# Kernel tuning notes

Measured on AMD Instinct MI355X. Metric: run time of the kernel, lower is better.

## Reference

```python
import jax, jax.numpy as jnp
import numpy as np

B, N, DIM = 4, 1024, 1024
HEADS, DH = 16, 64
INNER = HEADS * DH          # 1024
PROJ_H = max(16, DH // 8)   # 16
TOP_K = 256
TEMP = 1.0
SCALE = DH ** -0.5
LN_EPS = 1e-5


def setup_inputs() -> dict:
    key = jax.random.key(0)
    ks = jax.random.split(key, 9)
    s = 0.02
    return {
        "x": jax.random.normal(ks[0], (B, N, DIM), dtype=jnp.float32),
        "w_qkv": jax.random.normal(ks[1], (3 * INNER, DIM), dtype=jnp.float32) * s,
        "w_out": jax.random.normal(ks[2], (DIM, INNER), dtype=jnp.float32) * s,
        "b_out": jnp.zeros((DIM,), dtype=jnp.float32),
        "ln_g": jnp.ones((DH,), dtype=jnp.float32),
        "ln_b": jnp.zeros((DH,), dtype=jnp.float32),
        "w1": jax.random.normal(ks[3], (PROJ_H, DH), dtype=jnp.float32) * s,
        "b1": jnp.zeros((PROJ_H,), dtype=jnp.float32),
        "w2": jax.random.normal(ks[4], (1, PROJ_H), dtype=jnp.float32) * s,
        "b2": jnp.zeros((1,), dtype=jnp.float32),
    }


def _soma_gate(token_feat, ln_g, ln_b, w1, b1, w2, b2):
    # token_feat: [B, N, DH] -> gate [B, N] in (0,1)
    mu = token_feat.mean(axis=-1, keepdims=True)
    var = token_feat.var(axis=-1, keepdims=True)
    H = (token_feat - mu) * jax.lax.rsqrt(var + LN_EPS) * ln_g + ln_b
    h = jax.nn.gelu(H @ w1.T + b1, approximate=False)
    scores = (h @ w2.T + b2)[..., 0]                       # [B, N]
    scores = scores / (TEMP + 1e-12)
    # top-k soft mask: non-topk positions set to -1e9 before sigmoid
    topk_vals, topk_idx = jax.lax.top_k(scores, TOP_K)
    b_idx = jnp.arange(scores.shape[0])[:, None]
    scores = jnp.full_like(scores, -1e9).at[b_idx, topk_idx].set(topk_vals)
    return jax.nn.sigmoid(scores)


def reference(x, w_qkv, w_out, b_out, ln_g, ln_b, w1, b1, w2, b2):
    Bx, Nx, _ = x.shape
    qkv = x @ w_qkv.T                                      # [B, N, 3*INNER]
    q, k, v = jnp.split(qkv, 3, axis=-1)
    to_heads = lambda t: t.reshape(Bx, Nx, HEADS, DH).transpose(0, 2, 1, 3)
    q, k, v = to_heads(q), to_heads(k), to_heads(v)        # [B, H, N, DH]

    dots = jnp.einsum('bhid,bhjd->bhij', q, k) * SCALE     # [B, H, N, N]

    q_mean = q.mean(axis=1)                                # [B, N, DH]
    gate = _soma_gate(q_mean, ln_g, ln_b, w1, b1, w2, b2)  # [B, N]
    dots = dots * (gate[:, None, :, None] * gate[:, None, None, :])

    attn = jax.nn.softmax(dots, axis=-1)
    out = jnp.einsum('bhij,bhjd->bhid', attn, v)           # [B, H, N, DH]
    out = out.transpose(0, 2, 1, 3).reshape(Bx, Nx, INNER)
    return out @ w_out.T + b_out
```

## Files before the change

### kernel.cpp

```cpp
#include <hip/hip_runtime.h>
#include <hip/hip_bf16.h>
#include <stdint.h>

typedef __bf16 bf16;
typedef __bf16 bf16x8 __attribute__((ext_vector_type(8)));
typedef float floatx4 __attribute__((ext_vector_type(4)));

typedef const __attribute__((address_space(1))) uint32_t glb_u32;
typedef __attribute__((address_space(3))) uint32_t lds_u32;

__device__ __forceinline__ void cp16(void* lds, const void* gp) {
    __builtin_amdgcn_global_load_lds((glb_u32*)gp, (lds_u32*)lds, 16, 0, 0);
}

#define MFMA16(a, b, c) __builtin_amdgcn_mfma_f32_16x16x32_bf16((a), (b), (c), 0, 0, 0)
#define SCALE_ 0.125f

__global__ __launch_bounds__(256) void k_cvt_prep(
    const float* __restrict__ x, const float* __restrict__ wq,
    const float* __restrict__ wo, bf16* __restrict__ xb,
    bf16* __restrict__ xl, bf16* __restrict__ wqb, bf16* __restrict__ wob,
    bf16* __restrict__ whl, float* __restrict__ xsum) {
    __shared__ float red[4][64];
    if (blockIdx.x < 4096) {
        size_t i8 = ((size_t)blockIdx.x * 256 + threadIdx.x) * 8;
        const float* src; bf16* dst; size_t off; bool isx = false;
        if (i8 < 4194304)      { src = x;  dst = xb;  off = i8; isx = true; }
        else if (i8 < 7340032) { src = wq; dst = wqb; off = i8 - 4194304; }
        else                   { src = wo; dst = wob; off = i8 - 7340032; }
        float4 a = *(const float4*)(src + off);
        float4 b = *(const float4*)(src + off + 4);
        union { bf16 h[8]; uint4 u; } hi, lo;
        hi.h[0] = (bf16)a.x; hi.h[1] = (bf16)a.y; hi.h[2] = (bf16)a.z; hi.h[3] = (bf16)a.w;
        hi.h[4] = (bf16)b.x; hi.h[5] = (bf16)b.y; hi.h[6] = (bf16)b.z; hi.h[7] = (bf16)b.w;
        *(uint4*)(dst + off) = hi.u;
        if (isx) {
            lo.h[0] = (bf16)(a.x - (float)hi.h[0]);
            lo.h[1] = (bf16)(a.y - (float)hi.h[1]);
            lo.h[2] = (bf16)(a.z - (float)hi.h[2]);
            lo.h[3] = (bf16)(a.w - (float)hi.h[3]);
            lo.h[4] = (bf16)(b.x - (float)hi.h[4]);
            lo.h[5] = (bf16)(b.y - (float)hi.h[5]);
            lo.h[6] = (bf16)(b.z - (float)hi.h[6]);
            lo.h[7] = (bf16)(b.w - (float)hi.h[7]);
            *(uint4*)(xl + off) = lo.u;
        }
    } else if (blockIdx.x < 4352) {
        int t = (blockIdx.x - 4096) * 256 + threadIdx.x;
        int k = t & 1023, d = t >> 10;
        float s = 0.f;
        #pragma unroll
        for (int h = 0; h < 16; ++h) s += wq[(size_t)(h * 64 + d) * 1024 + k];
        s *= (1.f / 16.f);
        bf16 hi = (bf16)s;
        whl[(size_t)d * 1024 + k] = hi;
        whl[(size_t)(64 + d) * 1024 + k] = (bf16)(s - (float)hi);
    } else {
        int j = blockIdx.x - 4352;
        int b = j >> 4, c0 = (j & 15) << 6;
        int lane = threadIdx.x & 63, q = threadIdx.x >> 6;
        const float* p = x + (size_t)b * 1048576 + (size_t)q * 262144 + c0 + lane;
        float s = 0.f;
        #pragma unroll 8
        for (int n = 0; n < 256; ++n) s += p[(size_t)n * 1024];
        red[q][lane] = s;
        __syncthreads();
        if (threadIdx.x < 64)
            xsum[b * 1024 + c0 + threadIdx.x] =
                red[0][threadIdx.x] + red[1][threadIdx.x] +
                red[2][threadIdx.x] + red[3][threadIdx.x];
    }
}

__global__ __launch_bounds__(256) void k_score_gemm(
    const bf16* __restrict__ xh, const bf16* __restrict__ xl,
    const bf16* __restrict__ whl, float* __restrict__ qm8) {
    __shared__ bf16 Ah[64 * 32];
    __shared__ bf16 Al[64 * 32];
    __shared__ bf16 Bs[128 * 32];
    const int t = threadIdx.x;
    const int lane = t & 63;
    const int w = t >> 6;
    const int m0 = (blockIdx.x >> 3) * 64;
    const int kbase = (blockIdx.x & 7) * 128;
    const int srow = t >> 2;
    const int scol = (t & 3) * 8;
    const int fr = lane & 15;
    const int kc = (lane >> 4) * 8;

    floatx4 zero4 = {0.f, 0.f, 0.f, 0.f};
    floatx4 acc[4] = {zero4, zero4, zero4, zero4};

    for (int k0 = kbase; k0 < kbase + 128; k0 += 32) {
        __syncthreads();
        cp16(Ah + t * 8,        xh + (size_t)(m0 + srow) * 1024 + k0 + scol);
        cp16(Al + t * 8,        xl + (size_t)(m0 + srow) * 1024 + k0 + scol);
        cp16(Bs + t * 8,        whl + (size_t)srow * 1024 + k0 + scol);
        cp16(Bs + t * 8 + 2048, whl + (size_t)(srow + 64) * 1024 + k0 + scol);
        __syncthreads();
        bf16x8 ah, al, bh[4], bl[4];
        ah = *(const bf16x8*)&Ah[(w * 16 + fr) * 32 + kc];
        al = *(const bf16x8*)&Al[(w * 16 + fr) * 32 + kc];
        #pragma unroll
        for (int ni = 0; ni < 4; ++ni) {
            bh[ni] = *(const bf16x8*)&Bs[(ni * 16 + fr) * 32 + kc];
            bl[ni] = *(const bf16x8*)&Bs[(64 + ni * 16 + fr) * 32 + kc];
        }
        #pragma unroll
        for (int ni = 0; ni < 4; ++ni) {
            acc[ni] = MFMA16(ah, bh[ni], acc[ni]);
            acc[ni] = MFMA16(ah, bl[ni], acc[ni]);
            acc[ni] = MFMA16(al, bh[ni], acc[ni]);
        }
    }

    const int rowb = (lane >> 4) * 4;
    const size_t kofs = (size_t)(blockIdx.x & 7) * 4096;
    #pragma unroll
    for (int ni = 0; ni < 4; ++ni)
        #pragma unroll
        for (int r = 0; r < 4; ++r)
            qm8[(kofs + m0 + w * 16 + rowb + r) * 64 + ni * 16 + fr] = acc[ni][r];
}

__global__ __launch_bounds__(256) void k_score_tail(
    const float* __restrict__ qm8, const float* __restrict__ lng,
    const float* __restrict__ lnb, const float* __restrict__ w1f,
    const float* __restrict__ b1f, const float* __restrict__ w2f,
    const float* __restrict__ b2f, float* __restrict__ scores) {
    const int w = threadIdx.x >> 6, lane = threadIdx.x & 63;
    const int r = blockIdx.x * 4 + w;
    __shared__ float Hs[4][64];
    __shared__ float hh[4][16];

    float qm = 0.f;
    #pragma unroll
    for (int ks = 0; ks < 8; ++ks)
        qm += qm8[((size_t)ks * 4096 + r) * 64 + lane];
    float s = qm;
    #pragma unroll
    for (int off = 32; off > 0; off >>= 1) s += __shfl_xor(s, off);
    float mu = s * (1.f / 64.f);
    float dx = qm - mu;
    float v2 = dx * dx;
    #pragma unroll
    for (int off = 32; off > 0; off >>= 1) v2 += __shfl_xor(v2, off);
    float var = v2 * (1.f / 64.f);
    float H = dx * (1.0f / sqrtf(var + 1e-5f)) * lng[lane] + lnb[lane];
    Hs[w][lane] = H;
    if (lane < 16) {
        float a = b1f[lane];
        #pragma unroll
        for (int d = 0; d < 64; ++d) a += Hs[w][d] * w1f[lane * 64 + d];
        hh[w][lane] = 0.5f * a * (1.0f + erff(a * 0.70710678118654752f));
    }
    if (lane == 0) {
        float sc = b2f[0];
        #pragma unroll
        for (int p = 0; p < 16; ++p) sc += hh[w][p] * w2f[p];
        scores[r] = sc;
    }
}

__global__ __launch_bounds__(256) void k_topk(const float* __restrict__ scores,
                                              float* __restrict__ gate,
                                              int* __restrict__ idx,
                                              float* __restrict__ gsel) {
    const int w = threadIdx.x >> 6, lane = threadIdx.x & 63;
    const float* sc = scores + w * 1024;
    float s[16];
    uint32_t key[16];
    #pragma unroll
    for (int i = 0; i < 16; ++i) {
        s[i] = sc[lane * 16 + i];
        uint32_t u = __float_as_uint(s[i]);
        key[i] = (u >> 31) ? ~u : (u | 0x80000000u);
    }
    uint32_t prefix = 0;
    for (int bit = 31; bit >= 0; --bit) {
        uint32_t cand = prefix | (1u << bit);
        int c = 0;
        #pragma unroll
        for (int i = 0; i < 16; ++i) c += (key[i] >= cand);
        #pragma unroll
        for (int off = 1; off < 64; off <<= 1) c += __shfl_xor(c, off);
        if (c >= 256) prefix = cand;
    }
    int cg = 0, eq = 0;
    #pragma unroll
    for (int i = 0; i < 16; ++i) { cg += (key[i] > prefix); eq += (key[i] == prefix); }
    #pragma unroll
    for (int off = 1; off < 64; off <<= 1) cg += __shfl_xor(cg, off);
    const int quota = 256 - cg;
    int xs = eq;
    #pragma unroll
    for (int off = 1; off < 64; off <<= 1) {
        int y = __shfl_up(xs, off);
        if (lane >= off) xs += y;
    }
    int run = xs - eq;
    bool selv[16];
    int cnt = 0;
    #pragma unroll
    for (int i = 0; i < 16; ++i) {
        bool sel = key[i] > prefix;
        if (key[i] == prefix) { sel = (run < quota); run++; }
        selv[i] = sel;
        cnt += sel ? 1 : 0;
        gate[w * 1024 + lane * 16 + i] = sel ? 1.0f / (1.0f + expf(-s[i])) : 0.0f;
    }
    int xc = cnt;
    #pragma unroll
    for (int off = 1; off < 64; off <<= 1) {
        int y = __shfl_up(xc, off);
        if (lane >= off) xc += y;
    }
    int pos = xc - cnt;
    #pragma unroll
    for (int i = 0; i < 16; ++i) {
        if (selv[i]) {
            idx[w * 256 + pos]  = lane * 16 + i;
            gsel[w * 256 + pos] = 1.0f / (1.0f + expf(-s[i]));
            pos++;
        }
    }
}

__global__ __launch_bounds__(256) void k_qkv_sel(
    const bf16* __restrict__ xb, const bf16* __restrict__ wqb,
    const int* __restrict__ idx, bf16* __restrict__ qsel,
    bf16* __restrict__ ksel, bf16* __restrict__ VselT,
    const float* __restrict__ xsum, float* __restrict__ meanVbuf) {
    __shared__ bf16 As[64 * 32];
    __shared__ bf16 Bs[128 * 32];
    __shared__ float xsS[1024];
    const int t = threadIdx.x;

    if (blockIdx.x >= 384) {
        const int j = blockIdx.x - 384, b = j >> 2, kq = j & 3;
        for (int k = t; k < 1024; k += 256) xsS[k] = xsum[b * 1024 + k];
        __syncthreads();
        const int k2 = kq * 256 + t;
        const bf16* wr = wqb + (size_t)(2048 + k2) * 1024;
        float s = 0.f;
        for (int k = 0; k < 1024; k += 8) {
            bf16x8 v = *(const bf16x8*)(wr + k);
            #pragma unroll
            for (int jj = 0; jj < 8; ++jj) s += (float)v[jj] * xsS[k + jj];
        }
        meanVbuf[b * 1024 + k2] = s * (1.f / 1024.f);
        return;
    }

    const int lane = t & 63;
    const int w = t >> 6;
    const int srow = t >> 2;
    const int scol = (t & 3) * 8;
    const int fr = lane & 15;
    const int kc = (lane >> 4) * 8;

    const int bid = blockIdx.x;
    const int n0 = (bid % 24) * 128;
    const int m0 = (bid / 24) * 64;
    const bf16* Bsrc = wqb + (size_t)n0 * 1024;
    const int mg1 = m0 + srow;
    const int tok1 = idx[(mg1 >> 8) * 256 + (mg1 & 255)];
    const size_t abase1 = ((size_t)(mg1 >> 8) * 1024 + tok1) * 1024;

    floatx4 zero4 = {0.f, 0.f, 0.f, 0.f};
    floatx4 acc[4][2];
    #pragma unroll
    for (int i = 0; i < 4; ++i)
        #pragma unroll
        for (int j = 0; j < 2; ++j) acc[i][j] = zero4;

    for (int k0 = 0; k0 < 1024; k0 += 32) {
        __syncthreads();
        cp16(As + t * 8,        xb + abase1 + k0 + scol);
        cp16(Bs + t * 8,        Bsrc + (size_t)srow * 1024 + k0 + scol);
        cp16(Bs + t * 8 + 2048, Bsrc + (size_t)(srow + 64) * 1024 + k0 + scol);
        __syncthreads();
        bf16x8 a[4], b[2];
        #pragma unroll
        for (int mi = 0; mi < 4; ++mi)
            a[mi] = *(const bf16x8*)&As[(mi * 16 + fr) * 32 + kc];
        #pragma unroll
        for (int ni = 0; ni < 2; ++ni)
            b[ni] = *(const bf16x8*)&Bs[(w * 32 + ni * 16 + fr) * 32 + kc];
        #pragma unroll
        for (int mi = 0; mi < 4; ++mi)
            #pragma unroll
            for (int ni = 0; ni < 2; ++ni)
                acc[mi][ni] = MFMA16(a[mi], b[ni], acc[mi][ni]);
    }

    const int rowb = (lane >> 4) * 4;
    #pragma unroll
    for (int ni = 0; ni < 2; ++ni) {
        const int n_base = n0 + w * 32 + ni * 16;
        const int region = n_base >> 10;
        const int nn = n_base & 1023;
        const int h = nn >> 6;
        const int dd = (nn & 63) + fr;
        if (region < 2) {
            #pragma unroll
            for (int mi = 0; mi < 4; ++mi)
                #pragma unroll
                for (int r = 0; r < 4; ++r) {
                    const int mg = m0 + mi * 16 + rowb + r;
                    const bf16 v = (bf16)acc[mi][ni][r];
                    if (region == 0) {
                        qsel[(size_t)mg * 1024 + h * 64 + dd] = v;
                    } else {
                        const int b = mg >> 8, s = mg & 255;
                        ksel[(((size_t)(b * 16 + h)) * 256 + s) * 64 + dd] = v;
                    }
                }
        } else {
            #pragma unroll
            for (int mi = 0; mi < 4; ++mi) {
                const int mgb = m0 + mi * 16 + rowb;
                const int b = mgb >> 8, s0 = mgb & 255;
                union { bf16 h4[4]; uint2 u; } pk;
                #pragma unroll
                for (int r = 0; r < 4; ++r) pk.h4[r] = (bf16)acc[mi][ni][r];
                *(uint2*)&VselT[(((size_t)(b * 16 + h)) * 64 + dd) * 256 + s0] = pk.u;
            }
        }
    }
}

__global__ __launch_bounds__(256) void k_attn(
    bf16* __restrict__ qsel, const bf16* __restrict__ Ksel,
    const bf16* __restrict__ VselT, const float* __restrict__ gsel,
    const float* __restrict__ meanVbuf, const bf16* __restrict__ wob,
    const float* __restrict__ b_out, float* __restrict__ ubase) {
    __shared__ bf16 Qs[64 * 72];
    __shared__ bf16 Ks[64 * 72];
    __shared__ bf16 Vs[64 * 72];
    __shared__ bf16 Ps[4][16 * 72];
    __shared__ float redS[4][64];
    __shared__ float SumV[64];
    __shared__ float mvS[1024];
    const int t = threadIdx.x;

    if (blockIdx.x >= 256) {
        const int j = blockIdx.x - 256, bb = j >> 2, nq = j & 3;
        for (int k = t; k < 1024; k += 256) mvS[k] = meanVbuf[bb * 1024 + k];
        __syncthreads();
        const int n = nq * 256 + t;
        const bf16* wr = wob + (size_t)n * 1024;
        float s = b_out[n];
        for (int k = 0; k < 1024; k += 8) {
            bf16x8 v = *(const bf16x8*)(wr + k);
            #pragma unroll
            for (int jj = 0; jj < 8; ++jj) s += (float)v[jj] * mvS[k + jj];
        }
        ubase[bb * 1024 + n] = s;
        return;
    }

    const int bh = blockIdx.x >> 2;
    const int qt = blockIdx.x & 3;
    const int b = bh >> 4, h = bh & 15;
    const int w = t >> 6, lane = t & 63;
    const int m0 = qt * 64;
    const bf16* kb = Ksel + (size_t)bh * 16384;
    const bf16* vb = VselT + (size_t)bh * 16384;

    #pragma unroll
    for (int c = 0; c < 2; ++c) {
        int idx2 = t + 256 * c, row = idx2 >> 3, c8 = (idx2 & 7) * 8;
        *(uint4*)&Qs[row * 72 + c8] =
            *(const uint4*)&qsel[(size_t)(b * 256 + m0 + row) * 1024 + h * 64 + c8];
    }
    {
        const int dd_ = t & 63, pp_ = t >> 6;
        const bf16* vr = vb + (size_t)dd_ * 256 + pp_ * 64;
        float ss = 0.f;
        #pragma unroll
        for (int k = 0; k < 64; k += 8) {
            bf16x8 v = *(const bf16x8*)(vr + k);
            #pragma unroll
            for (int jj = 0; jj < 8; ++jj) ss += (float)v[jj];
        }
        redS[pp_][dd_] = ss;
    }
    const int fr = lane & 15;
    const int kq = lane >> 4;
    const int rowb = kq * 4;
    __syncthreads();
    if (t < 64)
        SumV[t] = meanVbuf[b * 1024 + h * 64 + t] * 1024.f -
                  (redS[0][t] + redS[1][t] + redS[2][t] + redS[3][t]);
    bf16x8 aq[2];
    aq[0] = *(const bf16x8*)&Qs[(w * 16 + fr) * 72 + kq * 8];
    aq[1] = *(const bf16x8*)&Qs[(w * 16 + fr) * 72 + 32 + kq * 8];

    float gq[4];
    #pragma unroll
    for (int r = 0; r < 4; ++r)
        gq[r] = gsel[b * 256 + m0 + w * 16 + rowb + r] * SCALE_;

    float mrow[4] = {0.f, 0.f, 0.f, 0.f};
    float lrow[4] = {0.f, 0.f, 0.f, 0.f};
    floatx4 zero4 = {0.f, 0.f, 0.f, 0.f};
    floatx4 Of[4] = {zero4, zero4, zero4, zero4};

    for (int jt = 0; jt < 4; ++jt) {
        const int j0 = jt * 64;
        __syncthreads();
        #pragma unroll
        for (int c = 0; c < 2; ++c) {
            int idx2 = t + 256 * c, row = idx2 >> 3, c8 = (idx2 & 7) * 8;
            *(uint4*)&Ks[row * 72 + c8] = *(const uint4*)&kb[(size_t)(j0 + row) * 64 + c8];
            *(uint4*)&Vs[row * 72 + c8] = *(const uint4*)&vb[(size_t)row * 256 + j0 + c8];
        }
        __syncthreads();

        floatx4 S[4] = {zero4, zero4, zero4, zero4};
        #pragma unroll
        for (int ks = 0; ks < 2; ++ks) {
            #pragma unroll
            for (int ni = 0; ni < 4; ++ni) {
                bf16x8 bfr = *(const bf16x8*)&Ks[(ni * 16 + fr) * 72 + ks * 32 + kq * 8];
                S[ni] = MFMA16(aq[ks], bfr, S[ni]);
            }
        }
        float gk[4];
        #pragma unroll
        for (int ni = 0; ni < 4; ++ni) gk[ni] = gsel[b * 256 + j0 + ni * 16 + fr];

        float p[4][4], rmax[4] = {0.f, 0.f, 0.f, 0.f};
        #pragma unroll
        for (int ni = 0; ni < 4; ++ni)
            #pragma unroll
            for (int r = 0; r < 4; ++r) {
                float sv = S[ni][r] * (gq[r] * gk[ni]);
                p[ni][r] = sv;
                rmax[r] = fmaxf(rmax[r], sv);
            }
        #pragma unroll
        for (int r = 0; r < 4; ++r) {
            #pragma unroll
            for (int off = 1; off < 16; off <<= 1)
                rmax[r] = fmaxf(rmax[r], __shfl_xor(rmax[r], off));
        }
        float alpha[4], rsum[4] = {0.f, 0.f, 0.f, 0.f};
        #pragma unroll
        for (int r = 0; r < 4; ++r) {
            float mn = fmaxf(mrow[r], rmax[r]);
            alpha[r] = __expf(mrow[r] - mn);
            mrow[r] = mn;
        }
        #pragma unroll
        for (int ni = 0; ni < 4; ++ni)
            #pragma unroll
            for (int r = 0; r < 4; ++r) {
                float pv = __expf(p[ni][r] - mrow[r]);
                p[ni][r] = pv;
                rsum[r] += pv;
            }
        #pragma unroll
        for (int r = 0; r < 4; ++r) {
            #pragma unroll
            for (int off = 1; off < 16; off <<= 1) rsum[r] += __shfl_xor(rsum[r], off);
            lrow[r] = lrow[r] * alpha[r] + rsum[r];
        }
        #pragma unroll
        for (int nd = 0; nd < 4; ++nd)
            #pragma unroll
            for (int r = 0; r < 4; ++r) Of[nd][r] *= alpha[r];

        #pragma unroll
        for (int ni = 0; ni < 4; ++ni)
            #pragma unroll
            for (int r = 0; r < 4; ++r)
                Ps[w][(rowb + r) * 72 + ni * 16 + fr] = (bf16)p[ni][r];

        #pragma unroll
        for (int ks = 0; ks < 2; ++ks) {
            bf16x8 ap = *(const bf16x8*)&Ps[w][fr * 72 + ks * 32 + kq * 8];
            #pragma unroll
            for (int nd = 0; nd < 4; ++nd) {
                bf16x8 bv = *(const bf16x8*)&Vs[(nd * 16 + fr) * 72 + ks * 32 + kq * 8];
                Of[nd] = MFMA16(ap, bv, Of[nd]);
            }
        }
    }

    #pragma unroll
    for (int nd = 0; nd < 4; ++nd)
        #pragma unroll
        for (int r = 0; r < 4; ++r) {
            float em = __expf(-mrow[r]);
            float num = Of[nd][r] + em * SumV[nd * 16 + fr];
            float den = lrow[r] + 768.0f * em;
            qsel[(size_t)(b * 256 + m0 + w * 16 + rowb + r) * 1024 +
                 h * 64 + nd * 16 + fr] = (bf16)(num / den);
        }
}

__global__ __launch_bounds__(256) void k_out_gemm(
    const bf16* __restrict__ A, const bf16* __restrict__ wob,
    float* __restrict__ outP) {
    __shared__ bf16 As[64 * 32];
    __shared__ bf16 Bs[128 * 32];
    const int t = threadIdx.x;
    const int lane = t & 63;
    const int w = t >> 6;
    const int srow = t >> 2;
    const int scol = (t & 3) * 8;
    const int fr = lane & 15;
    const int kc = (lane >> 4) * 8;

    const int ks = blockIdx.x >> 7;
    const int rem = blockIdx.x & 127;
    const int m0 = (rem >> 3) * 64;
    const int n0 = (rem & 7) * 128;
    const int kbase = ks * 512;
    const bf16* Bsrc = wob + (size_t)n0 * 1024;

    floatx4 zero4 = {0.f, 0.f, 0.f, 0.f};
    floatx4 acc[4][2];
    #pragma unroll
    for (int i = 0; i < 4; ++i)
        #pragma unroll
        for (int j = 0; j < 2; ++j) acc[i][j] = zero4;

    for (int k0 = kbase; k0 < kbase + 512; k0 += 32) {
        __syncthreads();
        cp16(As + t * 8,        A + (size_t)(m0 + srow) * 1024 + k0 + scol);
        cp16(Bs + t * 8,        Bsrc + (size_t)srow * 1024 + k0 + scol);
        cp16(Bs + t * 8 + 2048, Bsrc + (size_t)(srow + 64) * 1024 + k0 + scol);
        __syncthreads();
        bf16x8 a[4], b[2];
        #pragma unroll
        for (int mi = 0; mi < 4; ++mi)
            a[mi] = *(const bf16x8*)&As[(mi * 16 + fr) * 32 + kc];
        #pragma unroll
        for (int ni = 0; ni < 2; ++ni)
            b[ni] = *(const bf16x8*)&Bs[(w * 32 + ni * 16 + fr) * 32 + kc];
        #pragma unroll
        for (int mi = 0; mi < 4; ++mi)
            #pragma unroll
            for (int ni = 0; ni < 2; ++ni)
                acc[mi][ni] = MFMA16(a[mi], b[ni], acc[mi][ni]);
    }

    const int rowb = (lane >> 4) * 4;
    float* dst = outP + (size_t)ks * 1048576;
    #pragma unroll
    for (int ni = 0; ni < 2; ++ni) {
        const int ng = n0 + w * 32 + ni * 16 + fr;
        #pragma unroll
        for (int mi = 0; mi < 4; ++mi)
            #pragma unroll
            for (int r = 0; r < 4; ++r) {
                const int mg = m0 + mi * 16 + rowb + r;
                dst[(size_t)mg * 1024 + ng] = acc[mi][ni][r];
            }
    }
}

__global__ __launch_bounds__(256) void k_out_red(
    const float* __restrict__ outP, const float* __restrict__ b_out,
    const int* __restrict__ idx, const float* __restrict__ ubase,
    const float* __restrict__ gate, float* __restrict__ out) {
    const int t = threadIdx.x, gb = blockIdx.x;
    if (gb < 1024) {
        const int mg = gb;
        const int c = t * 4;
        float4 v0 = *(const float4*)(outP + (size_t)mg * 1024 + c);
        float4 v1 = *(const float4*)(outP + 1048576 + (size_t)mg * 1024 + c);
        float4 bb = *(const float4*)(b_out + c);
        float4 r;
        r.x = v0.x + v1.x + bb.x;
        r.y = v0.y + v1.y + bb.y;
        r.z = v0.z + v1.z + bb.z;
        r.w = v0.w + v1.w + bb.w;
        const int b = mg >> 8, s = mg & 255;
        const int tok = idx[b * 256 + s];
        *(float4*)(out + ((size_t)b * 1024 + tok) * 1024 + c) = r;
    } else {
        const int fb = gb - 1024;
        const int c = t * 4;
        #pragma unroll
        for (int r = 0; r < 4; ++r) {
            const int tokg = fb * 4 + r;
            if (gate[tokg] > 0.f) continue;
            const int b = tokg >> 10;
            *(float4*)(out + (size_t)tokg * 1024 + c) =
                *(const float4*)(ubase + b * 1024 + c);
        }
    }
}

extern "C" void kernel_launch(void* const* d_in, const int* in_sizes, int n_in,
                              void* d_out, int out_size, void* d_ws, size_t ws_size,
                              hipStream_t stream) {
    const float* x     = (const float*)d_in[0];
    const float* w_qkv = (const float*)d_in[1];
    const float* w_out = (const float*)d_in[2];
    const float* b_out = (const float*)d_in[3];
    const float* ln_g  = (const float*)d_in[4];
    const float* ln_b  = (const float*)d_in[5];
    const float* w1    = (const float*)d_in[6];
    const float* b1    = (const float*)d_in[7];
    const float* w2    = (const float*)d_in[8];
    const float* b2    = (const float*)d_in[9];
    float* out = (float*)d_out;

    char* ws = (char*)d_ws;
    bf16*  qsel  = (bf16*)(ws);
    bf16*  ksel  = (bf16*)(ws + 4194304);
    bf16*  VselT = (bf16*)(ws + 6291456);
    float* qm8   = (float*)(ws);
    float* xsum  = (float*)(ws + 8388608);
    bf16*  xb    = (bf16*)(ws + 16777216);
    float* outP  = (float*)(ws + 16777216);
    bf16*  wqb   = (bf16*)(ws + 25165824);
    bf16*  wob   = (bf16*)(ws + 31457280);
    int*   idx      = (int*)(ws + 33554432);
    float* gsel     = (float*)(ws + 33558528);
    float* scores   = (float*)(ws + 33562624);
    float* gate     = (float*)(ws + 33579008);
    float* meanVbuf = (float*)(ws + 33595392);
    float* ubase    = (float*)(ws + 33611776);
    bf16*  whl      = (bf16*)(ws + 33685504);
    bf16*  xlbuf    = (bf16*)(ws + 35651584);

    k_cvt_prep<<<4416, 256, 0, stream>>>(x, w_qkv, w_out, xb, xlbuf, wqb, wob, whl, xsum);
    k_score_gemm<<<512, 256, 0, stream>>>(xb, xlbuf, whl, qm8);
    k_score_tail<<<1024, 256, 0, stream>>>(qm8, ln_g, ln_b, w1, b1, w2, b2, scores);
    k_topk<<<1, 256, 0, stream>>>(scores, gate, idx, gsel);
    k_qkv_sel<<<400, 256, 0, stream>>>(xb, wqb, idx, qsel, ksel, VselT, xsum, meanVbuf);
    k_attn<<<272, 256, 0, stream>>>(qsel, ksel, VselT, gsel, meanVbuf, wob, b_out, ubase);
    k_out_gemm<<<256, 256, 0, stream>>>(qsel, wob, outP);
    k_out_red<<<2048, 256, 0, stream>>>(outP, b_out, idx, ubase, gate, out);
}
```

Baseline: 198.8 us.

## Fuse score GEMM, score tail and top-k into one kernel with grid barriers

Merges three kernels (score GEMM, LayerNorm/MLP score tail, top-k selection) into one persistent kernel of 512 blocks that uses a software grid barrier built on an atomic counter. The counter is reset in the preceding prep kernel. The aim is to remove two kernel launches and the idle gaps between small dependent stages. The cost is that all 512 blocks must be co-resident for the spin barrier to avoid deadlock, which the launch bounds hint of two blocks per CU is meant to support. Only block 0 then runs top-k while the rest exit.

```diff
diff --git a/kernel.cpp b/kernel.cpp
--- a/kernel.cpp
+++ b/kernel.cpp
@@ -15,12 +15,24 @@
 
 #define MFMA16(a, b, c) __builtin_amdgcn_mfma_f32_16x16x32_bf16((a), (b), (c), 0, 0, 0)
 #define SCALE_ 0.125f
+
+__device__ __forceinline__ void grid_barrier(int* cnt, int target) {
+    __syncthreads();
+    if (threadIdx.x == 0) {
+        __threadfence();
+        __hip_atomic_fetch_add(cnt, 1, __ATOMIC_RELAXED, __HIP_MEMORY_SCOPE_AGENT);
+        while (__hip_atomic_load(cnt, __ATOMIC_RELAXED, __HIP_MEMORY_SCOPE_AGENT) < target)
+            __builtin_amdgcn_s_sleep(2);
+        __threadfence();
+    }
+    __syncthreads();
+}
 
 __global__ __launch_bounds__(256) void k_cvt_prep(
     const float* __restrict__ x, const float* __restrict__ wq,
     const float* __restrict__ wo, bf16* __restrict__ xb,
     bf16* __restrict__ xl, bf16* __restrict__ wqb, bf16* __restrict__ wob,
-    bf16* __restrict__ whl, float* __restrict__ xsum) {
+    bf16* __restrict__ whl, float* __restrict__ xsum, int* __restrict__ sync_cnt) {
     __shared__ float red[4][64];
     if (blockIdx.x < 4096) {
         size_t i8 = ((size_t)blockIdx.x * 256 + threadIdx.x) * 8;
@@ -57,6 +69,7 @@
         whl[(size_t)(64 + d) * 1024 + k] = (bf16)(s - (float)hi);
     } else {
         int j = blockIdx.x - 4352;
+        if (j == 0 && threadIdx.x == 0) *sync_cnt = 0;
         int b = j >> 4, c0 = (j & 15) << 6;
         int lane = threadIdx.x & 63, q = threadIdx.x >> 6;
         const float* p = x + (size_t)b * 1048576 + (size_t)q * 262144 + c0 + lane;
@@ -72,156 +85,161 @@
     }
 }
 
-__global__ __launch_bounds__(256) void k_score_gemm(
+__global__ __launch_bounds__(256, 2) void k_score_fused(
     const bf16* __restrict__ xh, const bf16* __restrict__ xl,
-    const bf16* __restrict__ whl, float* __restrict__ qm8) {
+    const bf16* __restrict__ whl, float* __restrict__ qm8,
+    const float* __restrict__ lng, const float* __restrict__ lnb,
+    const float* __restrict__ w1f, const float* __restrict__ b1f,
+    const float* __restrict__ w2f, const float* __restrict__ b2f,
+    float* __restrict__ scores, float* __restrict__ gate,
+    int* __restrict__ idxo, float* __restrict__ gsel,
+    int* __restrict__ sync_cnt) {
     __shared__ bf16 Ah[64 * 32];
     __shared__ bf16 Al[64 * 32];
     __shared__ bf16 Bs[128 * 32];
+    __shared__ float Hs[4][64];
+    __shared__ float hh[4][16];
     const int t = threadIdx.x;
     const int lane = t & 63;
     const int w = t >> 6;
-    const int m0 = (blockIdx.x >> 3) * 64;
-    const int kbase = (blockIdx.x & 7) * 128;
-    const int srow = t >> 2;
-    const int scol = (t & 3) * 8;
-    const int fr = lane & 15;
-    const int kc = (lane >> 4) * 8;
-
-    floatx4 zero4 = {0.f, 0.f, 0.f, 0.f};
-    floatx4 acc[4] = {zero4, zero4, zero4, zero4};
-
-    for (int k0 = kbase; k0 < kbase + 128; k0 += 32) {
-        __syncthreads();
-        cp16(Ah + t * 8,        xh + (size_t)(m0 + srow) * 1024 + k0 + scol);
-        cp16(Al + t * 8,        xl + (size_t)(m0 + srow) * 1024 + k0 + scol);
-        cp16(Bs + t * 8,        whl + (size_t)srow * 1024 + k0 + scol);
-        cp16(Bs + t * 8 + 2048, whl + (size_t)(srow + 64) * 1024 + k0 + scol);
-        __syncthreads();
-        bf16x8 ah, al, bh[4], bl[4];
-        ah = *(const bf16x8*)&Ah[(w * 16 + fr) * 32 + kc];
-        al = *(const bf16x8*)&Al[(w * 16 + fr) * 32 + kc];
-        #pragma unroll
-        for (int ni = 0; ni < 4; ++ni) {
-            bh[ni] = *(const bf16x8*)&Bs[(ni * 16 + fr) * 32 + kc];
-            bl[ni] = *(const bf16x8*)&Bs[(64 + ni * 16 + fr) * 32 + kc];
-        }
-        #pragma unroll
-        for (int ni = 0; ni < 4; ++ni) {
-            acc[ni] = MFMA16(ah, bh[ni], acc[ni]);
-            acc[ni] = MFMA16(ah, bl[ni], acc[ni]);
-            acc[ni] = MFMA16(al, bh[ni], acc[ni]);
-        }
-    }
-
-    const int rowb = (lane >> 4) * 4;
-    const size_t kofs = (size_t)(blockIdx.x & 7) * 4096;
-    #pragma unroll
-    for (int ni = 0; ni < 4; ++ni)
-        #pragma unroll
-        for (int r = 0; r < 4; ++r)
-            qm8[(kofs + m0 + w * 16 + rowb + r) * 64 + ni * 16 + fr] = acc[ni][r];
-}
-
-__global__ __launch_bounds__(256) void k_score_tail(
-    const float* __restrict__ qm8, const float* __restrict__ lng,
-    const float* __restrict__ lnb, const float* __restrict__ w1f,
-    const float* __restrict__ b1f, const float* __restrict__ w2f,
-    const float* __restrict__ b2f, float* __restrict__ scores) {
-    const int w = threadIdx.x >> 6, lane = threadIdx.x & 63;
-    const int r = blockIdx.x * 4 + w;
-    __shared__ float Hs[4][64];
-    __shared__ float hh[4][16];
-
-    float qm = 0.f;
-    #pragma unroll
-    for (int ks = 0; ks < 8; ++ks)
-        qm += qm8[((size_t)ks * 4096 + r) * 64 + lane];
-    float s = qm;
-    #pragma unroll
-    for (int off = 32; off > 0; off >>= 1) s += __shfl_xor(s, off);
-    float mu = s * (1.f / 64.f);
-    float dx = qm - mu;
-    float v2 = dx * dx;
-    #pragma unroll
-    for (int off = 32; off > 0; off >>= 1) v2 += __shfl_xor(v2, off);
-    float var = v2 * (1.f / 64.f);
-    float H = dx * (1.0f / sqrtf(var + 1e-5f)) * lng[lane] + lnb[lane];
-    Hs[w][lane] = H;
-    if (lane < 16) {
-        float a = b1f[lane];
-        #pragma unroll
-        for (int d = 0; d < 64; ++d) a += Hs[w][d] * w1f[lane * 64 + d];
-        hh[w][lane] = 0.5f * a * (1.0f + erff(a * 0.70710678118654752f));
-    }
-    if (lane == 0) {
-        float sc = b2f[0];
-        #pragma unroll
-        for (int p = 0; p < 16; ++p) sc += hh[w][p] * w2f[p];
-        scores[r] = sc;
-    }
-}
-
-__global__ __launch_bounds__(256) void k_topk(const float* __restrict__ scores,
-                                              float* __restrict__ gate,
-                                              int* __restrict__ idx,
-                                              float* __restrict__ gsel) {
-    const int w = threadIdx.x >> 6, lane = threadIdx.x & 63;
-    const float* sc = scores + w * 1024;
-    float s[16];
-    uint32_t key[16];
-    #pragma unroll
-    for (int i = 0; i < 16; ++i) {
-        s[i] = sc[lane * 16 + i];
-        uint32_t u = __float_as_uint(s[i]);
-        key[i] = (u >> 31) ? ~u : (u | 0x80000000u);
-    }
-    uint32_t prefix = 0;
-    for (int bit = 31; bit >= 0; --bit) {
-        uint32_t cand = prefix | (1u << bit);
-        int c = 0;
-        #pragma unroll
-        for (int i = 0; i < 16; ++i) c += (key[i] >= cand);
-        #pragma unroll
-        for (int off = 1; off < 64; off <<= 1) c += __shfl_xor(c, off);
-        if (c >= 256) prefix = cand;
-    }
-    int cg = 0, eq = 0;
-    #pragma unroll
-    for (int i = 0; i < 16; ++i) { cg += (key[i] > prefix); eq += (key[i] == prefix); }
-    #pragma unroll
-    for (int off = 1; off < 64; off <<= 1) cg += __shfl_xor(cg, off);
-    const int quota = 256 - cg;
-    int xs = eq;
-    #pragma unroll
-    for (int off = 1; off < 64; off <<= 1) {
-        int y = __shfl_up(xs, off);
-        if (lane >= off) xs += y;
-    }
-    int run = xs - eq;
-    bool selv[16];
-    int cnt = 0;
-    #pragma unroll
-    for (int i = 0; i < 16; ++i) {
-        bool sel = key[i] > prefix;
-        if (key[i] == prefix) { sel = (run < quota); run++; }
-        selv[i] = sel;
-        cnt += sel ? 1 : 0;
-        gate[w * 1024 + lane * 16 + i] = sel ? 1.0f / (1.0f + expf(-s[i])) : 0.0f;
-    }
-    int xc = cnt;
-    #pragma unroll
-    for (int off = 1; off < 64; off <<= 1) {
-        int y = __shfl_up(xc, off);
-        if (lane >= off) xc += y;
-    }
-    int pos = xc - cnt;
-    #pragma unroll
-    for (int i = 0; i < 16; ++i) {
-        if (selv[i]) {
-            idx[w * 256 + pos]  = lane * 16 + i;
-            gsel[w * 256 + pos] = 1.0f / (1.0f + expf(-s[i]));
-            pos++;
+
+    {
+        const int m0 = (blockIdx.x >> 3) * 64;
+        const int kbase = (blockIdx.x & 7) * 128;
+        const int srow = t >> 2;
+        const int scol = (t & 3) * 8;
+        const int fr = lane & 15;
+        const int kc = (lane >> 4) * 8;
+
+        floatx4 zero4 = {0.f, 0.f, 0.f, 0.f};
+        floatx4 acc[4] = {zero4, zero4, zero4, zero4};
+
+        for (int k0 = kbase; k0 < kbase + 128; k0 += 32) {
+            __syncthreads();
+            cp16(Ah + t * 8,        xh + (size_t)(m0 + srow) * 1024 + k0 + scol);
+            cp16(Al + t * 8,        xl + (size_t)(m0 + srow) * 1024 + k0 + scol);
+            cp16(Bs + t * 8,        whl + (size_t)srow * 1024 + k0 + scol);
+            cp16(Bs + t * 8 + 2048, whl + (size_t)(srow + 64) * 1024 + k0 + scol);
+            __syncthreads();
+            bf16x8 ah, al, bh[4], bl[4];
+            ah = *(const bf16x8*)&Ah[(w * 16 + fr) * 32 + kc];
+            al = *(const bf16x8*)&Al[(w * 16 + fr) * 32 + kc];
+            #pragma unroll
+            for (int ni = 0; ni < 4; ++ni) {
+                bh[ni] = *(const bf16x8*)&Bs[(ni * 16 + fr) * 32 + kc];
+                bl[ni] = *(const bf16x8*)&Bs[(64 + ni * 16 + fr) * 32 + kc];
+            }
+            #pragma unroll
+            for (int ni = 0; ni < 4; ++ni) {
+                acc[ni] = MFMA16(ah, bh[ni], acc[ni]);
+                acc[ni] = MFMA16(ah, bl[ni], acc[ni]);
+                acc[ni] = MFMA16(al, bh[ni], acc[ni]);
+            }
+        }
+
+        const int rowb = (lane >> 4) * 4;
+        const size_t kofs = (size_t)(blockIdx.x & 7) * 4096;
+        #pragma unroll
+        for (int ni = 0; ni < 4; ++ni)
+            #pragma unroll
+            for (int r = 0; r < 4; ++r)
+                qm8[(kofs + m0 + w * 16 + rowb + r) * 64 + ni * 16 + fr] = acc[ni][r];
+    }
+
+    grid_barrier(sync_cnt, 512);
+
+    #pragma unroll
+    for (int g = 0; g < 2; ++g) {
+        const int r = blockIdx.x * 8 + g * 4 + w;
+        float qm = 0.f;
+        #pragma unroll
+        for (int ks = 0; ks < 8; ++ks)
+            qm += qm8[((size_t)ks * 4096 + r) * 64 + lane];
+        float s = qm;
+        #pragma unroll
+        for (int off = 32; off > 0; off >>= 1) s += __shfl_xor(s, off);
+        float mu = s * (1.f / 64.f);
+        float dx = qm - mu;
+        float v2 = dx * dx;
+        #pragma unroll
+        for (int off = 32; off > 0; off >>= 1) v2 += __shfl_xor(v2, off);
+        float var = v2 * (1.f / 64.f);
+        float H = dx * (1.0f / sqrtf(var + 1e-5f)) * lng[lane] + lnb[lane];
+        Hs[w][lane] = H;
+        if (lane < 16) {
+            float a = b1f[lane];
+            #pragma unroll
+            for (int d = 0; d < 64; ++d) a += Hs[w][d] * w1f[lane * 64 + d];
+            hh[w][lane] = 0.5f * a * (1.0f + erff(a * 0.70710678118654752f));
+        }
+        if (lane == 0) {
+            float sc = b2f[0];
+            #pragma unroll
+            for (int p = 0; p < 16; ++p) sc += hh[w][p] * w2f[p];
+            scores[r] = sc;
+        }
+    }
+
+    grid_barrier(sync_cnt, 1024);
+
+    if (blockIdx.x != 0) return;
+    {
+        const float* sc = scores + w * 1024;
+        float s[16];
+        uint32_t key[16];
+        #pragma unroll
+        for (int i = 0; i < 16; ++i) {
+            s[i] = sc[lane * 16 + i];
+            uint32_t u = __float_as_uint(s[i]);
+            key[i] = (u >> 31) ? ~u : (u | 0x80000000u);
+        }
+        uint32_t prefix = 0;
+        for (int bit = 31; bit >= 0; --bit) {
+            uint32_t cand = prefix | (1u << bit);
+            int c = 0;
+            #pragma unroll
+            for (int i = 0; i < 16; ++i) c += (key[i] >= cand);
+            #pragma unroll
+            for (int off = 1; off < 64; off <<= 1) c += __shfl_xor(c, off);
+            if (c >= 256) prefix = cand;
+        }
+        int cg = 0, eq = 0;
+        #pragma unroll
+        for (int i = 0; i < 16; ++i) { cg += (key[i] > prefix); eq += (key[i] == prefix); }
+        #pragma unroll
+        for (int off = 1; off < 64; off <<= 1) cg += __shfl_xor(cg, off);
+        const int quota = 256 - cg;
+        int xs = eq;
+        #pragma unroll
+        for (int off = 1; off < 64; off <<= 1) {
+            int y = __shfl_up(xs, off);
+            if (lane >= off) xs += y;
+        }
+        int run = xs - eq;
+        bool selv[16];
+        int cnt = 0;
+        #pragma unroll
+        for (int i = 0; i < 16; ++i) {
+            bool sel = key[i] > prefix;
+            if (key[i] == prefix) { sel = (run < quota); run++; }
+            selv[i] = sel;
+            cnt += sel ? 1 : 0;
+            gate[w * 1024 + lane * 16 + i] = sel ? 1.0f / (1.0f + expf(-s[i])) : 0.0f;
+        }
+        int xc = cnt;
+        #pragma unroll
+        for (int off = 1; off < 64; off <<= 1) {
+            int y = __shfl_up(xc, off);
+            if (lane >= off) xc += y;
+        }
+        int pos = xc - cnt;
+        #pragma unroll
+        for (int i = 0; i < 16; ++i) {
+            if (selv[i]) {
+                idxo[w * 256 + pos]  = lane * 16 + i;
+                gsel[w * 256 + pos] = 1.0f / (1.0f + expf(-s[i]));
+                pos++;
+            }
         }
     }
 }
@@ -617,6 +635,7 @@
     bf16*  VselT = (bf16*)(ws + 6291456);
     float* qm8   = (float*)(ws);
     float* xsum  = (float*)(ws + 8388608);
+    int*   sync_cnt = (int*)(ws + 8404992);
     bf16*  xb    = (bf16*)(ws + 16777216);
     float* outP  = (float*)(ws + 16777216);
     bf16*  wqb   = (bf16*)(ws + 25165824);
@@ -630,10 +649,11 @@
     bf16*  whl      = (bf16*)(ws + 33685504);
     bf16*  xlbuf    = (bf16*)(ws + 35651584);
 
-    k_cvt_prep<<<4416, 256, 0, stream>>>(x, w_qkv, w_out, xb, xlbuf, wqb, wob, whl, xsum);
-    k_score_gemm<<<512, 256, 0, stream>>>(xb, xlbuf, whl, qm8);
-    k_score_tail<<<1024, 256, 0, stream>>>(qm8, ln_g, ln_b, w1, b1, w2, b2, scores);
-    k_topk<<<1, 256, 0, stream>>>(scores, gate, idx, gsel);
+    k_cvt_prep<<<4416, 256, 0, stream>>>(x, w_qkv, w_out, xb, xlbuf, wqb, wob,
+                                         whl, xsum, sync_cnt);
+    k_score_fused<<<512, 256, 0, stream>>>(xb, xlbuf, whl, qm8, ln_g, ln_b,
+                                           w1, b1, w2, b2, scores, gate, idx,
+                                           gsel, sync_cnt);
     k_qkv_sel<<<400, 256, 0, stream>>>(xb, wqb, idx, qsel, ksel, VselT, xsum, meanVbuf);
     k_attn<<<272, 256, 0, stream>>>(qsel, ksel, VselT, gsel, meanVbuf, wob, b_out, ubase);
     k_out_gemm<<<256, 256, 0, stream>>>(qsel, wob, outP);
```

Measured after the change: 284.6 us. 43.2% more time.

## Fuse top-k into score tail via last-block atomic and shrink QKV-select tiles

Applied to the files above, without the earlier changes.

Removes the separate single-block top-k kernel: the score-tail kernel counts finished blocks with an agent-scope atomic, and the last block runs the radix top-k selection. The counter is reset inside the prep kernel. Separately, the selected-token QKV GEMM tile height drops from 64 to 32 rows, doubling the grid from 384 to 768 GEMM blocks for better CU occupancy, at the cost of more B-tile reloads. The fused path depends on the atomic counter and memory fences being correct.

```diff
diff --git a/kernel.cpp b/kernel.cpp
--- a/kernel.cpp
+++ b/kernel.cpp
@@ -20,7 +20,7 @@
     const float* __restrict__ x, const float* __restrict__ wq,
     const float* __restrict__ wo, bf16* __restrict__ xb,
     bf16* __restrict__ xl, bf16* __restrict__ wqb, bf16* __restrict__ wob,
-    bf16* __restrict__ whl, float* __restrict__ xsum) {
+    bf16* __restrict__ whl, float* __restrict__ xsum, int* __restrict__ sync_cnt) {
     __shared__ float red[4][64];
     if (blockIdx.x < 4096) {
         size_t i8 = ((size_t)blockIdx.x * 256 + threadIdx.x) * 8;
@@ -57,6 +57,7 @@
         whl[(size_t)(64 + d) * 1024 + k] = (bf16)(s - (float)hi);
     } else {
         int j = blockIdx.x - 4352;
+        if (j == 0 && threadIdx.x == 0) *sync_cnt = 0;
         int b = j >> 4, c0 = (j & 15) << 6;
         int lane = threadIdx.x & 63, q = threadIdx.x >> 6;
         const float* p = x + (size_t)b * 1048576 + (size_t)q * 262144 + c0 + lane;
@@ -127,11 +128,14 @@
     const float* __restrict__ qm8, const float* __restrict__ lng,
     const float* __restrict__ lnb, const float* __restrict__ w1f,
     const float* __restrict__ b1f, const float* __restrict__ w2f,
-    const float* __restrict__ b2f, float* __restrict__ scores) {
+    const float* __restrict__ b2f, float* __restrict__ scores,
+    float* __restrict__ gate, int* __restrict__ idxo,
+    float* __restrict__ gsel, int* __restrict__ sync_cnt) {
     const int w = threadIdx.x >> 6, lane = threadIdx.x & 63;
     const int r = blockIdx.x * 4 + w;
     __shared__ float Hs[4][64];
     __shared__ float hh[4][16];
+    __shared__ int isLast;
 
     float qm = 0.f;
     #pragma unroll
@@ -160,68 +164,75 @@
         for (int p = 0; p < 16; ++p) sc += hh[w][p] * w2f[p];
         scores[r] = sc;
     }
-}
-
-__global__ __launch_bounds__(256) void k_topk(const float* __restrict__ scores,
-                                              float* __restrict__ gate,
-                                              int* __restrict__ idx,
-                                              float* __restrict__ gsel) {
-    const int w = threadIdx.x >> 6, lane = threadIdx.x & 63;
-    const float* sc = scores + w * 1024;
-    float s[16];
-    uint32_t key[16];
-    #pragma unroll
-    for (int i = 0; i < 16; ++i) {
-        s[i] = sc[lane * 16 + i];
-        uint32_t u = __float_as_uint(s[i]);
-        key[i] = (u >> 31) ? ~u : (u | 0x80000000u);
-    }
-    uint32_t prefix = 0;
-    for (int bit = 31; bit >= 0; --bit) {
-        uint32_t cand = prefix | (1u << bit);
-        int c = 0;
-        #pragma unroll
-        for (int i = 0; i < 16; ++i) c += (key[i] >= cand);
-        #pragma unroll
-        for (int off = 1; off < 64; off <<= 1) c += __shfl_xor(c, off);
-        if (c >= 256) prefix = cand;
-    }
-    int cg = 0, eq = 0;
-    #pragma unroll
-    for (int i = 0; i < 16; ++i) { cg += (key[i] > prefix); eq += (key[i] == prefix); }
-    #pragma unroll
-    for (int off = 1; off < 64; off <<= 1) cg += __shfl_xor(cg, off);
-    const int quota = 256 - cg;
-    int xs = eq;
-    #pragma unroll
-    for (int off = 1; off < 64; off <<= 1) {
-        int y = __shfl_up(xs, off);
-        if (lane >= off) xs += y;
-    }
-    int run = xs - eq;
-    bool selv[16];
-    int cnt = 0;
-    #pragma unroll
-    for (int i = 0; i < 16; ++i) {
-        bool sel = key[i] > prefix;
-        if (key[i] == prefix) { sel = (run < quota); run++; }
-        selv[i] = sel;
-        cnt += sel ? 1 : 0;
-        gate[w * 1024 + lane * 16 + i] = sel ? 1.0f / (1.0f + expf(-s[i])) : 0.0f;
-    }
-    int xc = cnt;
-    #pragma unroll
-    for (int off = 1; off < 64; off <<= 1) {
-        int y = __shfl_up(xc, off);
-        if (lane >= off) xc += y;
-    }
-    int pos = xc - cnt;
-    #pragma unroll
-    for (int i = 0; i < 16; ++i) {
-        if (selv[i]) {
-            idx[w * 256 + pos]  = lane * 16 + i;
-            gsel[w * 256 + pos] = 1.0f / (1.0f + expf(-s[i]));
-            pos++;
+
+    __syncthreads();
+    if (threadIdx.x == 0) {
+        __threadfence();
+        int old = __hip_atomic_fetch_add(sync_cnt, 1, __ATOMIC_ACQ_REL,
+                                         __HIP_MEMORY_SCOPE_AGENT);
+        isLast = (old == 1023);
+    }
+    __syncthreads();
+    if (!isLast) return;
+    __threadfence();
+
+    {
+        const float* sc = scores + w * 1024;
+        float sv[16];
+        uint32_t key[16];
+        #pragma unroll
+        for (int i = 0; i < 16; ++i) {
+            sv[i] = sc[lane * 16 + i];
+            uint32_t u = __float_as_uint(sv[i]);
+            key[i] = (u >> 31) ? ~u : (u | 0x80000000u);
+        }
+        uint32_t prefix = 0;
+        for (int bit = 31; bit >= 0; --bit) {
+            uint32_t cand = prefix | (1u << bit);
+            int c = 0;
+            #pragma unroll
+            for (int i = 0; i < 16; ++i) c += (key[i] >= cand);
+            #pragma unroll
+            for (int off = 1; off < 64; off <<= 1) c += __shfl_xor(c, off);
+            if (c >= 256) prefix = cand;
+        }
+        int cg = 0, eq = 0;
+        #pragma unroll
+        for (int i = 0; i < 16; ++i) { cg += (key[i] > prefix); eq += (key[i] == prefix); }
+        #pragma unroll
+        for (int off = 1; off < 64; off <<= 1) cg += __shfl_xor(cg, off);
+        const int quota = 256 - cg;
+        int xs = eq;
+        #pragma unroll
+        for (int off = 1; off < 64; off <<= 1) {
+            int y = __shfl_up(xs, off);
+            if (lane >= off) xs += y;
+        }
+        int run = xs - eq;
+        bool selv[16];
+        int cnt = 0;
+        #pragma unroll
+        for (int i = 0; i < 16; ++i) {
+            bool sel = key[i] > prefix;
+            if (key[i] == prefix) { sel = (run < quota); run++; }
+            selv[i] = sel;
+            cnt += sel ? 1 : 0;
+            gate[w * 1024 + lane * 16 + i] = sel ? 1.0f / (1.0f + expf(-sv[i])) : 0.0f;
+        }
+        int xc = cnt;
+        #pragma unroll
+        for (int off = 1; off < 64; off <<= 1) {
+            int y = __shfl_up(xc, off);
+            if (lane >= off) xc += y;
+        }
+        int pos = xc - cnt;
+        #pragma unroll
+        for (int i = 0; i < 16; ++i) {
+            if (selv[i]) {
+                idxo[w * 256 + pos] = lane * 16 + i;
+                gsel[w * 256 + pos] = 1.0f / (1.0f + expf(-sv[i]));
+                pos++;
+            }
         }
     }
 }
@@ -231,13 +242,13 @@
     const int* __restrict__ idx, bf16* __restrict__ qsel,
     bf16* __restrict__ ksel, bf16* __restrict__ VselT,
     const float* __restrict__ xsum, float* __restrict__ meanVbuf) {
-    __shared__ bf16 As[64 * 32];
+    __shared__ bf16 As[32 * 32];
     __shared__ bf16 Bs[128 * 32];
     __shared__ float xsS[1024];
     const int t = threadIdx.x;
 
-    if (blockIdx.x >= 384) {
-        const int j = blockIdx.x - 384, b = j >> 2, kq = j & 3;
+    if (blockIdx.x >= 768) {
+        const int j = blockIdx.x - 768, b = j >> 2, kq = j & 3;
         for (int k = t; k < 1024; k += 256) xsS[k] = xsum[b * 1024 + k];
         __syncthreads();
         const int k2 = kq * 256 + t;
@@ -261,34 +272,37 @@
 
     const int bid = blockIdx.x;
     const int n0 = (bid % 24) * 128;
-    const int m0 = (bid / 24) * 64;
+    const int m0 = (bid / 24) * 32;
     const bf16* Bsrc = wqb + (size_t)n0 * 1024;
-    const int mg1 = m0 + srow;
-    const int tok1 = idx[(mg1 >> 8) * 256 + (mg1 & 255)];
-    const size_t abase1 = ((size_t)(mg1 >> 8) * 1024 + tok1) * 1024;
+    size_t abase1 = 0;
+    if (t < 128) {
+        const int mg1 = m0 + srow;
+        const int tok1 = idx[(mg1 >> 8) * 256 + (mg1 & 255)];
+        abase1 = ((size_t)(mg1 >> 8) * 1024 + tok1) * 1024;
+    }
 
     floatx4 zero4 = {0.f, 0.f, 0.f, 0.f};
-    floatx4 acc[4][2];
-    #pragma unroll
-    for (int i = 0; i < 4; ++i)
+    floatx4 acc[2][2];
+    #pragma unroll
+    for (int i = 0; i < 2; ++i)
         #pragma unroll
         for (int j = 0; j < 2; ++j) acc[i][j] = zero4;
 
     for (int k0 = 0; k0 < 1024; k0 += 32) {
         __syncthreads();
-        cp16(As + t * 8,        xb + abase1 + k0 + scol);
+        if (t < 128) cp16(As + t * 8, xb + abase1 + k0 + scol);
         cp16(Bs + t * 8,        Bsrc + (size_t)srow * 1024 + k0 + scol);
         cp16(Bs + t * 8 + 2048, Bsrc + (size_t)(srow + 64) * 1024 + k0 + scol);
         __syncthreads();
-        bf16x8 a[4], b[2];
-        #pragma unroll
-        for (int mi = 0; mi < 4; ++mi)
+        bf16x8 a[2], b[2];
+        #pragma unroll
+        for (int mi = 0; mi < 2; ++mi)
             a[mi] = *(const bf16x8*)&As[(mi * 16 + fr) * 32 + kc];
         #pragma unroll
         for (int ni = 0; ni < 2; ++ni)
             b[ni] = *(const bf16x8*)&Bs[(w * 32 + ni * 16 + fr) * 32 + kc];
         #pragma unroll
-        for (int mi = 0; mi < 4; ++mi)
+        for (int mi = 0; mi < 2; ++mi)
             #pragma unroll
             for (int ni = 0; ni < 2; ++ni)
                 acc[mi][ni] = MFMA16(a[mi], b[ni], acc[mi][ni]);
@@ -304,7 +318,7 @@
         const int dd = (nn & 63) + fr;
         if (region < 2) {
             #pragma unroll
-            for (int mi = 0; mi < 4; ++mi)
+            for (int mi = 0; mi < 2; ++mi)
                 #pragma unroll
                 for (int r = 0; r < 4; ++r) {
                     const int mg = m0 + mi * 16 + rowb + r;
@@ -318,7 +332,7 @@
                 }
         } else {
             #pragma unroll
-            for (int mi = 0; mi < 4; ++mi) {
+            for (int mi = 0; mi < 2; ++mi) {
                 const int mgb = m0 + mi * 16 + rowb;
                 const int b = mgb >> 8, s0 = mgb & 255;
                 union { bf16 h4[4]; uint2 u; } pk;
@@ -617,6 +631,7 @@
     bf16*  VselT = (bf16*)(ws + 6291456);
     float* qm8   = (float*)(ws);
     float* xsum  = (float*)(ws + 8388608);
+    int*   sync_cnt = (int*)(ws + 8404992);
     bf16*  xb    = (bf16*)(ws + 16777216);
     float* outP  = (float*)(ws + 16777216);
     bf16*  wqb   = (bf16*)(ws + 25165824);
@@ -630,11 +645,12 @@
     bf16*  whl      = (bf16*)(ws + 33685504);
     bf16*  xlbuf    = (bf16*)(ws + 35651584);
 
-    k_cvt_prep<<<4416, 256, 0, stream>>>(x, w_qkv, w_out, xb, xlbuf, wqb, wob, whl, xsum);
+    k_cvt_prep<<<4416, 256, 0, stream>>>(x, w_qkv, w_out, xb, xlbuf, wqb, wob,
+                                         whl, xsum, sync_cnt);
     k_score_gemm<<<512, 256, 0, stream>>>(xb, xlbuf, whl, qm8);
-    k_score_tail<<<1024, 256, 0, stream>>>(qm8, ln_g, ln_b, w1, b1, w2, b2, scores);
-    k_topk<<<1, 256, 0, stream>>>(scores, gate, idx, gsel);
-    k_qkv_sel<<<400, 256, 0, stream>>>(xb, wqb, idx, qsel, ksel, VselT, xsum, meanVbuf);
+    k_score_tail<<<1024, 256, 0, stream>>>(qm8, ln_g, ln_b, w1, b1, w2, b2,
+                                           scores, gate, idx, gsel, sync_cnt);
+    k_qkv_sel<<<784, 256, 0, stream>>>(xb, wqb, idx, qsel, ksel, VselT, xsum, meanVbuf);
     k_attn<<<272, 256, 0, stream>>>(qsel, ksel, VselT, gsel, meanVbuf, wob, b_out, ubase);
     k_out_gemm<<<256, 256, 0, stream>>>(qsel, wob, outP);
     k_out_red<<<2048, 256, 0, stream>>>(outP, b_out, idx, ubase, gate, out);
```

New measurement: 238.0 us. 1.2x slower.
